# Kernel optimization log

Measured on AMD Instinct MI355X. Metric: run time of the kernel, lower is better.

The kernel has to match this reference:

```python
import jax, jax.numpy as jnp
import numpy as np

T, B, M = 512, 4096, 2
DT = 1.0
HARD_RESET = True


def setup_inputs() -> dict:
    key = jax.random.key(0)
    ks = jax.random.split(key, 8)
    x_seq = jax.random.normal(ks[0], (T, B), jnp.float32) * 0.5
    w = jax.random.normal(ks[1], (B, B), jnp.float32) * (0.5 / np.sqrt(B))
    b = jax.random.normal(ks[2], (B,), jnp.float32) * 0.1
    v0 = jnp.zeros((B,), jnp.float32)
    Iasc0 = jnp.zeros((B, M), jnp.float32)
    v_th = jnp.ones((B,), jnp.float32)
    v_reset = jnp.zeros((B,), jnp.float32)
    v_rest = jnp.zeros((B,), jnp.float32)
    c_m = jnp.ones((B,), jnp.float32)
    tau = jax.random.uniform(ks[3], (B,), jnp.float32, 5.0, 20.0)
    k = jax.random.uniform(ks[4], (B, M), jnp.float32, 0.1, 0.5)
    asc = jax.random.normal(ks[5], (B, M), jnp.float32) * 0.1
    mask = jnp.ones((B,), jnp.float32)
    return dict(x_seq=x_seq, w=w, b=b, v0=v0, Iasc0=Iasc0, v_th=v_th,
                v_reset=v_reset, v_rest=v_rest, c_m=c_m, tau=tau, k=k,
                asc=asc, mask=mask)


def reference(x_seq, w, b, v0, Iasc0, v_th, v_reset, v_rest, c_m, tau, k, asc, mask):
    a = jnp.exp(-DT / tau)                 # (B,) voltage decay
    bdec = jnp.exp(-k * DT)                # (B,M) ASC decay

    def step(carry, x_t):
        v, I, s_prev = carry
        I_sum = I.sum(-1)                  # (B,)
        lin = w @ s_prev                   # recurrent GEMV against prev spikes
        x = x_t + b + lin
        v_inf = v_rest + tau * (x + I_sum) / c_m
        v_p = v_inf + (v - v_inf) * a
        u = (v_p - v_th) / (v_th - v_reset)
        s = (u > 0.0).astype(v_p.dtype) * mask
        if HARD_RESET:
            v_post = v_p - (v_p - v_reset) * s
        else:
            v_post = v_p - (v_th - v_reset) * s
        I_new = I * bdec + asc * s[:, None]
        return (v_post, I_new, s), (s, v_post)

    (v_fin, I_fin, _), (s_seq, v_seq) = jax.lax.scan(
        step, (v0, Iasc0, jnp.zeros_like(v0)), x_seq)
    return s_seq, v_seq, v_fin, I_fin
```

## Files before the change

### kernel.cpp

```cpp
#include <hip/hip_runtime.h>
#include <math.h>

#define TSTEPS 512
#define BN 4096
#define NBLK 64
#define NTHR 576
#define NPB 64
#define NGW 8
#define ESTRIDE 16

typedef unsigned long long u64;

__device__ __forceinline__ u64 ld_agent(const u64* p) {
    return __hip_atomic_load(p, __ATOMIC_RELAXED, __HIP_MEMORY_SCOPE_AGENT);
}
__device__ __forceinline__ void st_agent(u64* p, u64 v) {
    __hip_atomic_store(p, v, __ATOMIC_RELAXED, __HIP_MEMORY_SCOPE_AGENT);
}
__device__ __forceinline__ void st_flag(unsigned* p, unsigned v) {
    __hip_atomic_store(p, v, __ATOMIC_RELEASE, __HIP_MEMORY_SCOPE_WORKGROUP);
}
__device__ __forceinline__ unsigned ld_flag(const unsigned* p) {
    return __hip_atomic_load(p, __ATOMIC_ACQUIRE, __HIP_MEMORY_SCOPE_WORKGROUP);
}

template<bool TR>
__global__ __launch_bounds__(NTHR, 1)
void glif_kernel(const float* __restrict__ x_seq, const float* __restrict__ w,
                 const float* __restrict__ b_in, const float* __restrict__ v0,
                 const float* __restrict__ Ia0, const float* __restrict__ vth_in,
                 const float* __restrict__ vrst_in, const float* __restrict__ vrest_in,
                 const float* __restrict__ cm_in, const float* __restrict__ tau_in,
                 const float* __restrict__ k_in, const float* __restrict__ asc_in,
                 const float* __restrict__ mask_in,
                 float* __restrict__ out_s, float* __restrict__ out_v,
                 float* __restrict__ out_vf, float* __restrict__ out_if,
                 u64* __restrict__ sbuf, unsigned* __restrict__ bar,
                 float* __restrict__ wT)
{
    __shared__ float    tile[64][65];
    __shared__ int      wlist[NGW][512];
    __shared__ float4   partials[4][NGW][16];
    __shared__ unsigned flags[NGW];

    const int blk = blockIdx.x;
    const int tid = threadIdx.x;
    const int n0 = blk * NPB;
    const int wv = tid >> 6;
    const int ln = tid & 63;

    if (TR) {
        for (int tt = 0; tt < 64; ++tt) {
            int tile_id = blk + tt * NBLK;
            int ti = tile_id >> 6, tj = tile_id & 63;
            if (tid < 512) {
                int c = tid & 63, r0 = tid >> 6;
#pragma unroll
                for (int rr = 0; rr < 8; ++rr) {
                    int r = r0 + rr * 8;
                    tile[r][c] = w[(size_t)(ti * 64 + r) * BN + tj * 64 + c];
                }
            }
            __syncthreads();
            if (tid < 512) {
                int rw = tid & 63, c0 = tid >> 6;
#pragma unroll
                for (int cc = 0; cc < 8; ++cc) {
                    int cw = c0 + cc * 8;
                    float mcol = mask_in[tj * 64 + cw];
                    wT[(size_t)(tj * 64 + cw) * BN + ti * 64 + rw] = tile[rw][cw] * mcol;
                }
            }
            __syncthreads();
        }
    }

    if (tid < NGW) flags[tid] = 0;

    __syncthreads();
    if (tid == 0) {
        __threadfence();
        __hip_atomic_fetch_add(bar, 1u, __ATOMIC_ACQ_REL, __HIP_MEMORY_SCOPE_AGENT);
        while (__hip_atomic_load(bar, __ATOMIC_RELAXED, __HIP_MEMORY_SCOPE_AGENT) < NBLK) {
            __builtin_amdgcn_s_sleep(8);
        }
        __threadfence();
    }
    __syncthreads();

    if (wv == 0) {
        const int n = n0 + ln;
        float v, I0, I1, bb, aa, bd0, bd1, as0, as1, vth, vrst, vrest, cm, tau, msk;
        v = v0[n]; I0 = Ia0[2 * n]; I1 = Ia0[2 * n + 1];
        bb = b_in[n]; vth = vth_in[n]; vrst = vrst_in[n]; vrest = vrest_in[n];
        cm = cm_in[n]; tau = tau_in[n]; msk = mask_in[n];
        aa  = (float)exp((double)(-1.0f / tau));
        bd0 = (float)exp((double)(-k_in[2 * n]));
        bd1 = (float)exp((double)(-k_in[2 * n + 1]));
        as0 = asc_in[2 * n]; as1 = asc_in[2 * n + 1];

        for (int t = 0; t < TSTEPS; ++t) {
            float xt = x_seq[(size_t)t * BN + n];

            if (ln < NGW) {
                const unsigned want = (unsigned)(t + 1);
                while (ld_flag(&flags[ln]) < want) {}
            }
            const float* pf = reinterpret_cast<const float*>(&partials[t & 3][0][0]);
            float l0 = pf[ln],        l1 = pf[64 + ln],  l2 = pf[128 + ln], l3 = pf[192 + ln];
            float l4 = pf[256 + ln],  l5 = pf[320 + ln], l6 = pf[384 + ln], l7 = pf[448 + ln];
            float lin = ((l0 + l1) + (l2 + l3)) + ((l4 + l5) + (l6 + l7));
            float xx = (xt + bb) + lin;
            float Isum = I0 + I1;
            float vinf = vrest + (tau * (xx + Isum)) / cm;
            float vp = vinf + (v - vinf) * aa;
            float uu = (vp - vth) / (vth - vrst);
            float s = (uu > 0.0f) ? msk : 0.0f;
            u64 bal = __ballot(s != 0.0f);
            u64 tagw = ((u64)(t + 1)) << 32;
            u64* dst = sbuf + ((size_t)((t + 1) & 1) * NBLK + blk) * ESTRIDE;
            if (ln < 2) st_agent(dst + ln, tagw | (u64)(unsigned)(bal >> (32 * ln)));
            float vpost = vp - (vp - vrst) * s;
            I0 = I0 * bd0 + as0 * s;
            I1 = I1 * bd1 + as1 * s;
            v = vpost;
            out_s[(size_t)t * BN + n] = s;
            out_v[(size_t)t * BN + n] = vpost;
        }
        out_vf[n] = v;
        out_if[2 * n] = I0;
        out_if[2 * n + 1] = I1;
    } else {
        const int gw = wv - 1;
        const int e = ln >> 3;
        const int sub = ln & 7;
        const int wsel = sub >> 2;
        const int bshift = 8 * (sub & 3);
        const int entry = gw * 8 + e;
        const int cbase = (entry << 6) + (sub << 3);
        const int cslot = ln >> 4, l16 = ln & 15;
        const float* wb4 = wT + n0 + l16 * 4;

        for (int t = 0; t < TSTEPS; ++t) {
            const u64* p = sbuf + ((size_t)(t & 1) * NBLK + entry) * ESTRIDE + wsel;
            const unsigned want = (unsigned)t;
            u64 ev;
            for (;;) {
                u64 A = ld_agent(p);
                u64 B = ld_agent(p);
                if ((unsigned)(A >> 32) == want) { ev = A; break; }
                if ((unsigned)(B >> 32) == want) { ev = B; break; }
            }
            unsigned byte = ((unsigned)ev >> bshift) & 0xFFu;

            int c = __popc(byte);
            int x = c;
#pragma unroll
            for (int d = 1; d < 64; d <<= 1) {
                int y = __shfl_up(x, d);
                if (ln >= d) x += y;
            }
            const int kw = __shfl(x, 63);
            int base = x - c;
            while (byte) { int bp = __ffs(byte) - 1; byte &= byte - 1; wlist[gw][base++] = cbase + bp; }

            if (TR) {
                float4 acc = make_float4(0.f, 0.f, 0.f, 0.f);
                const int R = (kw + 3) >> 2;
                for (int r = 0; r < R; r += 8) {
#pragma unroll
                    for (int u = 0; u < 8; ++u) {
                        int idx = (r + u) * 4 + cslot;
                        bool pg = idx < kw;
                        int j = wlist[gw][pg ? idx : 0];
                        float m = pg ? 1.0f : 0.0f;
                        const float4 wvv = *reinterpret_cast<const float4*>(wb4 + ((size_t)j << 12));
                        acc.x = fmaf(wvv.x, m, acc.x);
                        acc.y = fmaf(wvv.y, m, acc.y);
                        acc.z = fmaf(wvv.z, m, acc.z);
                        acc.w = fmaf(wvv.w, m, acc.w);
                    }
                }
#pragma unroll
                for (int d = 16; d < 64; d <<= 1) {
                    acc.x += __shfl_xor(acc.x, d);
                    acc.y += __shfl_xor(acc.y, d);
                    acc.z += __shfl_xor(acc.z, d);
                    acc.w += __shfl_xor(acc.w, d);
                }
                if (ln < 16) partials[t & 3][gw][ln] = acc;
            } else {
                float accs = 0.f;
                const float* wrow = w + (size_t)(n0 + ln) * BN;
                for (int i = 0; i < kw; ++i) {
                    int j = wlist[gw][i];
                    accs = fmaf(wrow[j], mask_in[j], accs);
                }
                reinterpret_cast<float*>(&partials[t & 3][gw][0])[ln] = accs;
            }
            if (ln == 0) st_flag(&flags[gw], (unsigned)(t + 1));
        }
    }
}

extern "C" void kernel_launch(void* const* d_in, const int* in_sizes, int n_in,
                              void* d_out, int out_size, void* d_ws, size_t ws_size,
                              hipStream_t stream)
{
    const float* x_seq = (const float*)d_in[0];
    const float* w     = (const float*)d_in[1];
    const float* b     = (const float*)d_in[2];
    const float* v0    = (const float*)d_in[3];
    const float* Ia0   = (const float*)d_in[4];
    const float* vth   = (const float*)d_in[5];
    const float* vrst  = (const float*)d_in[6];
    const float* vrest = (const float*)d_in[7];
    const float* cm    = (const float*)d_in[8];
    const float* tau   = (const float*)d_in[9];
    const float* k     = (const float*)d_in[10];
    const float* asc   = (const float*)d_in[11];
    const float* mask  = (const float*)d_in[12];

    float* out_s  = (float*)d_out;
    float* out_v  = out_s + (size_t)TSTEPS * BN;
    float* out_vf = out_v + (size_t)TSTEPS * BN;
    float* out_if = out_vf + BN;

    const size_t mb_bytes = (size_t)2 * NBLK * ESTRIDE * sizeof(u64);
    u64* sbuf     = (u64*)d_ws;
    unsigned* bar = (unsigned*)((char*)d_ws + mb_bytes);
    float* wT     = (float*)((char*)d_ws + mb_bytes + 256);

    const size_t need = mb_bytes + 256 + (size_t)BN * BN * sizeof(float);
    const bool tr = (ws_size >= need);

    hipMemsetAsync(d_ws, 0, mb_bytes + 256, stream);

    if (tr) {
        glif_kernel<true><<<NBLK, NTHR, 0, stream>>>(
            x_seq, w, b, v0, Ia0, vth, vrst, vrest, cm, tau, k, asc, mask,
            out_s, out_v, out_vf, out_if, sbuf, bar, wT);
    } else {
        glif_kernel<false><<<NBLK, NTHR, 0, stream>>>(
            x_seq, w, b, v0, Ia0, vth, vrst, vrest, cm, tau, k, asc, mask,
            out_s, out_v, out_vf, out_if, sbuf, bar, (float*)w);
    }
}
```

Measured before the change: 1.656 ms.

## Process spike entries as they arrive instead of building compacted shared list

Each gather wave now polls its eight source-block spike entries together and, as soon as an entry's tag matches, accumulates the corresponding weight columns per lane directly, without the prefix-scan compaction into a shared index list. This removes the shared-memory list, the scan shuffles and the cross-lane float4 reduction, and lets work on early-arriving blocks overlap with waiting for late ones. In exchange each lane does scalar loads per spike (no float4) with divergent bit loops. The consumer wave also has every lane poll a flag instead of only eight lanes, and a waitcnt is added before publishing the flag.

```diff
diff --git a/kernel.cpp b/kernel.cpp
--- a/kernel.cpp
+++ b/kernel.cpp
@@ -39,8 +39,7 @@
                  float* __restrict__ wT)
 {
     __shared__ float    tile[64][65];
-    __shared__ int      wlist[NGW][512];
-    __shared__ float4   partials[4][NGW][16];
+    __shared__ float    partials[4][NGW][64];
     __shared__ unsigned flags[NGW];
 
     const int blk = blockIdx.x;
@@ -102,11 +101,12 @@
         for (int t = 0; t < TSTEPS; ++t) {
             float xt = x_seq[(size_t)t * BN + n];
 
-            if (ln < NGW) {
+            {
                 const unsigned want = (unsigned)(t + 1);
-                while (ld_flag(&flags[ln]) < want) {}
-            }
-            const float* pf = reinterpret_cast<const float*>(&partials[t & 3][0][0]);
+                const unsigned* fp = &flags[ln & 7];
+                while (ld_flag(fp) < want) {}
+            }
+            const float* pf = &partials[t & 3][0][0];
             float l0 = pf[ln],        l1 = pf[64 + ln],  l2 = pf[128 + ln], l3 = pf[192 + ln];
             float l4 = pf[256 + ln],  l5 = pf[320 + ln], l6 = pf[384 + ln], l7 = pf[448 + ln];
             float lin = ((l0 + l1) + (l2 + l3)) + ((l4 + l5) + (l6 + l7));
@@ -135,69 +135,57 @@
         const int e = ln >> 3;
         const int sub = ln & 7;
         const int wsel = sub >> 2;
-        const int bshift = 8 * (sub & 3);
         const int entry = gw * 8 + e;
-        const int cbase = (entry << 6) + (sub << 3);
-        const int cslot = ln >> 4, l16 = ln & 15;
-        const float* wb4 = wT + n0 + l16 * 4;
+        const float* wcol = wT + n0 + ln;
+        const float* wrow = w + (size_t)(n0 + ln) * BN;
 
         for (int t = 0; t < TSTEPS; ++t) {
             const u64* p = sbuf + ((size_t)(t & 1) * NBLK + entry) * ESTRIDE + wsel;
             const unsigned want = (unsigned)t;
-            u64 ev;
-            for (;;) {
-                u64 A = ld_agent(p);
-                u64 B = ld_agent(p);
-                if ((unsigned)(A >> 32) == want) { ev = A; break; }
-                if ((unsigned)(B >> 32) == want) { ev = B; break; }
-            }
-            unsigned byte = ((unsigned)ev >> bshift) & 0xFFu;
-
-            int c = __popc(byte);
-            int x = c;
-#pragma unroll
-            for (int d = 1; d < 64; d <<= 1) {
-                int y = __shfl_up(x, d);
-                if (ln >= d) x += y;
-            }
-            const int kw = __shfl(x, 63);
-            int base = x - c;
-            while (byte) { int bp = __ffs(byte) - 1; byte &= byte - 1; wlist[gw][base++] = cbase + bp; }
-
-            if (TR) {
-                float4 acc = make_float4(0.f, 0.f, 0.f, 0.f);
-                const int R = (kw + 3) >> 2;
-                for (int r = 0; r < R; r += 8) {
-#pragma unroll
-                    for (int u = 0; u < 8; ++u) {
-                        int idx = (r + u) * 4 + cslot;
-                        bool pg = idx < kw;
-                        int j = wlist[gw][pg ? idx : 0];
-                        float m = pg ? 1.0f : 0.0f;
-                        const float4 wvv = *reinterpret_cast<const float4*>(wb4 + ((size_t)j << 12));
-                        acc.x = fmaf(wvv.x, m, acc.x);
-                        acc.y = fmaf(wvv.y, m, acc.y);
-                        acc.z = fmaf(wvv.z, m, acc.z);
-                        acc.w = fmaf(wvv.w, m, acc.w);
-                    }
-                }
-#pragma unroll
-                for (int d = 16; d < 64; d <<= 1) {
-                    acc.x += __shfl_xor(acc.x, d);
-                    acc.y += __shfl_xor(acc.y, d);
-                    acc.z += __shfl_xor(acc.z, d);
-                    acc.w += __shfl_xor(acc.w, d);
-                }
-                if (ln < 16) partials[t & 3][gw][ln] = acc;
-            } else {
-                float accs = 0.f;
-                const float* wrow = w + (size_t)(n0 + ln) * BN;
-                for (int i = 0; i < kw; ++i) {
-                    int j = wlist[gw][i];
-                    accs = fmaf(wrow[j], mask_in[j], accs);
-                }
-                reinterpret_cast<float*>(&partials[t & 3][gw][0])[ln] = accs;
-            }
+            u64 ev = 0;
+            bool got = false;
+            unsigned pend = 0xFFu;
+            float a0 = 0.f, a1 = 0.f, a2 = 0.f, a3 = 0.f,
+                  a4 = 0.f, a5 = 0.f, a6 = 0.f, a7 = 0.f;
+
+            while (pend) {
+                if (!got) {
+                    ev = ld_agent(p);
+                    got = ((unsigned)(ev >> 32) == want);
+                }
+                const u64 rm = __ballot(got);
+                const unsigned evlo = (unsigned)ev;
+
+#define PROC_ENTRY(E2, ACC)                                                     \
+                if ((pend & (1u << E2)) &&                                      \
+                    (((rm >> (8 * E2)) & 0xFFull) == 0xFFull)) {                \
+                    pend &= ~(1u << E2);                                        \
+                    unsigned mlo = (unsigned)__shfl((int)evlo, 8 * E2);         \
+                    unsigned mhi = (unsigned)__shfl((int)evlo, 8 * E2 + 4);     \
+                    u64 mm = ((u64)mhi << 32) | (u64)mlo;                       \
+                    const int cb = ((gw << 3) + E2) << 6;                       \
+                    while (mm) {                                                \
+                        int bp = (int)__builtin_ctzll(mm);                      \
+                        mm &= mm - 1;                                           \
+                        if (TR) ACC += wcol[(size_t)(cb + bp) << 12];           \
+                        else    ACC += wrow[cb + bp] * mask_in[cb + bp];        \
+                    }                                                           \
+                }
+
+                PROC_ENTRY(0, a0)
+                PROC_ENTRY(1, a1)
+                PROC_ENTRY(2, a2)
+                PROC_ENTRY(3, a3)
+                PROC_ENTRY(4, a4)
+                PROC_ENTRY(5, a5)
+                PROC_ENTRY(6, a6)
+                PROC_ENTRY(7, a7)
+#undef PROC_ENTRY
+            }
+
+            float lp = ((a0 + a1) + (a2 + a3)) + ((a4 + a5) + (a6 + a7));
+            partials[t & 3][gw][ln] = lp;
+            __builtin_amdgcn_s_waitcnt(0);
             if (ln == 0) st_flag(&flags[gw], (unsigned)(t + 1));
         }
     }
```

Result: slower. 5.006 ms (+202.3%).
